# Performance work log

Measured on AMD Instinct MI355X. Metric: run time of the kernel, lower is better.

The kernel has to match this reference:

```python
import jax, jax.numpy as jnp
import numpy as np

N, E, D, H = 4096, 131072, 256, 8
HD = D // H
NEG_INF = -1e30  # stand-in for float('-inf'); avoids inf-inf NaN issues, softmax identical


def _linear(x, W, b):
    return x @ W + b


def setup_inputs() -> dict:
    key = jax.random.key(0)
    ks = jax.random.split(key, 16)
    s = 1.0 / np.sqrt(D)
    inp = {
        "x": jax.random.normal(ks[0], (N, D), jnp.float32),
        "edge_index": jax.random.randint(ks[1], (2, E), 0, N, jnp.int32),
        "edge_attr": jax.random.normal(ks[2], (E, D), jnp.float32),
        "Wq": jax.random.normal(ks[3], (D, D), jnp.float32) * s,
        "bq": jnp.zeros((D,), jnp.float32),
        "Wk": jax.random.normal(ks[4], (D, D), jnp.float32) * s,
        "bk": jnp.zeros((D,), jnp.float32),
        "Wv": jax.random.normal(ks[5], (D, D), jnp.float32) * s,
        "bv": jnp.zeros((D,), jnp.float32),
        "We": jax.random.normal(ks[6], (D, D), jnp.float32) * s,
        "be": jnp.zeros((D,), jnp.float32),
        "Wo": jax.random.normal(ks[7], (D, D), jnp.float32) * s,
        "bo": jnp.zeros((D,), jnp.float32),
        "Wi": jax.random.normal(ks[8], (D, D), jnp.float32) * s,
        "bi": jnp.zeros((D,), jnp.float32),
        "ln_g": jnp.ones((D,), jnp.float32),
        "ln_b": jnp.zeros((D,), jnp.float32),
    }
    return inp


def reference(x, edge_index, edge_attr, Wq, bq, Wk, bk, Wv, bv, We, be, Wo, bo, Wi, bi, ln_g, ln_b):
    n, e = x.shape[0], edge_attr.shape[0]
    Q = _linear(x, Wq, bq).reshape(n, H, HD)
    K = _linear(x, Wk, bk).reshape(n, H, HD)
    V = _linear(x, Wv, bv).reshape(n, H, HD)
    Efeat = _linear(edge_attr, We, be).reshape(e, H, HD)

    src, tgt = edge_index[0], edge_index[1]
    Q_src = Q[src]                     # (E, H, HD)
    K_tgt = K[tgt]                     # (E, H, HD)
    attn_edge = ((Q_src * K_tgt).sum(-1)
                 + (Q_src * Efeat).sum(-1)
                 + (Efeat * K_tgt).sum(-1)) / np.sqrt(HD)   # (E, H)

    attn_scores = jnp.full((n, n, H), NEG_INF, jnp.float32)
    attn_scores = attn_scores.at[src, tgt].set(attn_edge)
    attn_self = (Q * K).sum(-1) / np.sqrt(HD)               # (N, H)
    ar = jnp.arange(n)
    attn_scores = attn_scores.at[ar, ar].set(attn_self)

    attn_weights = jax.nn.softmax(attn_scores, axis=1)      # (N, N, H)
    # dropout in eval mode: identity
    node_out = jnp.einsum('ijh,jhd->ihd', attn_weights, V).reshape(n, -1)
    node_out = _linear(node_out, Wo, bo)

    x_proj = _linear(x, Wi, bi)
    h = x_proj + node_out
    mu = h.mean(-1, keepdims=True)
    var = ((h - mu) ** 2).mean(-1, keepdims=True)
    node_out = (h - mu) / jnp.sqrt(var + 1e-5) * ln_g + ln_b

    edge_out = _linear(edge_attr, We, be)
    return node_out, edge_out
```

## Files before the change

kernel.cpp:

```cpp
#include <hip/hip_runtime.h>

#define N_NODES 4096
#define N_EDGES 131072
#define DIM     256
#define HEADS   8
#define HDIM    32
#define MAXDEG  320
#define MAXDEGP 321

typedef unsigned short u16;
typedef unsigned int   u32;

using f32x4  = __attribute__((ext_vector_type(4))) float;
using bf16x8 = __attribute__((ext_vector_type(8))) short;
using u16x4  = __attribute__((ext_vector_type(4))) unsigned short;
using u16x8  = __attribute__((ext_vector_type(8))) unsigned short;

__device__ __forceinline__ u16 f2bf(float f) {
  u32 u = __float_as_uint(f);
  u += 0x7fffu + ((u >> 16) & 1u);
  return (u16)(u >> 16);
}
__device__ __forceinline__ float bf2f(u16 u) {
  return __uint_as_float(((u32)u) << 16);
}
__device__ __forceinline__ float dot4(float4 a, float4 b) {
  return a.x * b.x + a.y * b.y + a.z * b.z + a.w * b.w;
}

__global__ __launch_bounds__(256) void prep2_k(
    const float* __restrict__ Wq, const float* __restrict__ Wk,
    const float* __restrict__ Wv, const float* __restrict__ Wi,
    const float* __restrict__ We, const float* __restrict__ Wo,
    const float* __restrict__ bq, const float* __restrict__ bk,
    const float* __restrict__ bv, const float* __restrict__ bi,
    u16* __restrict__ WcatT, u16* __restrict__ WeT, u16* __restrict__ WoT,
    float* __restrict__ bcat, int* __restrict__ cursor)
{
  __shared__ float t[64][65];
  int b = blockIdx.x;
  int tid = threadIdx.x;
  if (b < 96) {
    int mat = b >> 4, tile = b & 15;
    int k0 = (tile >> 2) * 64, n0 = (tile & 3) * 64;
    const float* W = (mat == 0) ? Wq : (mat == 1) ? Wk : (mat == 2) ? Wv
                   : (mat == 3) ? Wi : (mat == 4) ? We : Wo;
    u16* dst; int nbase;
    if (mat < 4)      { dst = WcatT; nbase = mat * 256; }
    else if (mat == 4){ dst = WeT;   nbase = 0; }
    else              { dst = WoT;   nbase = 0; }
    int c = tid & 63, r0 = tid >> 6;
#pragma unroll
    for (int r = 0; r < 16; ++r) {
      int row = r0 + r * 4;
      t[row][c] = W[(size_t)(k0 + row) * 256 + n0 + c];
    }
    __syncthreads();
#pragma unroll
    for (int r = 0; r < 16; ++r) {
      int nn = r0 + r * 4;
      dst[(size_t)(nbase + n0 + nn) * 256 + k0 + c] = f2bf(t[c][nn]);
    }
  } else if (b == 96) {
#pragma unroll
    for (int j = 0; j < 4; ++j) {
      const float* bb = (j == 0) ? bq : (j == 1) ? bk : (j == 2) ? bv : bi;
      bcat[j * 256 + tid] = bb[tid];
    }
  } else {
    ((int4*)cursor)[(b - 97) * 256 + tid] = make_int4(0, 0, 0, 0);
  }
}

template<int MODE>
__device__ __forceinline__ void gemm_big_body(
    const float* __restrict__ A, const u16* __restrict__ BT,
    const float* __restrict__ bias, float* __restrict__ C, int Nn,
    int m0, int nc0,
    u16* __restrict__ Kb, u16* __restrict__ Vb,
    const float* __restrict__ QKVI, const float* __restrict__ lng,
    const float* __restrict__ lnb, float* __restrict__ outN,
    u16 (&As)[2][128 * 32], u16 (&Bs)[2][256 * 32])
{
  const int tid = threadIdx.x;
  const int w = tid >> 6, l = tid & 63;
  const int wr = w >> 2, wc = w & 3;
  const int fr = l & 15, hi = l >> 4;

  f32x4 pa[2];
  u16x8 pb[2];
  f32x4 acc[4][4] = {};

  auto loadstep = [&](int kt) {
#pragma unroll
    for (int i = 0; i < 2; ++i) {
      int j = tid + 512 * i;
      pa[i] = __builtin_nontemporal_load(
          (const f32x4*)(A + (size_t)(m0 + (j >> 3)) * 256 + kt * 32 + ((j & 7) << 2)));
    }
#pragma unroll
    for (int i = 0; i < 2; ++i) {
      int j = tid + 512 * i;
      pb[i] = *(const u16x8*)(BT + (size_t)(nc0 + (j >> 2)) * 256 + kt * 32 + ((j & 3) << 3));
    }
  };
  auto storestep = [&](int buf) {
#pragma unroll
    for (int i = 0; i < 2; ++i) {
      int j = tid + 512 * i;
      int row = j >> 3;
      int c16 = (j & 7) >> 1, half = j & 1;
      int swc = (c16 + ((row >> 1) & 3)) & 3;
      u16x4 u;
      u.x = f2bf(pa[i][0]); u.y = f2bf(pa[i][1]); u.z = f2bf(pa[i][2]); u.w = f2bf(pa[i][3]);
      *(u16x4*)&As[buf][row * 32 + swc * 8 + half * 4] = u;
    }
#pragma unroll
    for (int i = 0; i < 2; ++i) {
      int j = tid + 512 * i;
      int row = j >> 2;
      int swc = ((j & 3) + ((row >> 1) & 3)) & 3;
      *(u16x8*)&Bs[buf][row * 32 + swc * 8] = pb[i];
    }
  };

  loadstep(0);
  storestep(0);

#pragma unroll
  for (int kt = 0; kt < 8; ++kt) {
    if (kt < 7) loadstep(kt + 1);
    __builtin_amdgcn_sched_barrier(0);
    asm volatile("s_waitcnt lgkmcnt(0)" ::: "memory");
    __builtin_amdgcn_s_barrier();
    __builtin_amdgcn_sched_barrier(0);
    const int cur = kt & 1;
    bf16x8 a[4], b[4];
#pragma unroll
    for (int mi = 0; mi < 4; ++mi) {
      int rA = wr * 64 + mi * 16 + fr;
      int swc = (hi + ((rA >> 1) & 3)) & 3;
      a[mi] = *(const bf16x8*)&As[cur][rA * 32 + swc * 8];
    }
#pragma unroll
    for (int ni = 0; ni < 4; ++ni) {
      int rB = wc * 64 + ni * 16 + fr;
      int swc = (hi + ((rB >> 1) & 3)) & 3;
      b[ni] = *(const bf16x8*)&Bs[cur][rB * 32 + swc * 8];
    }
#pragma unroll
    for (int mi = 0; mi < 4; ++mi)
#pragma unroll
      for (int ni = 0; ni < 4; ++ni)
        acc[mi][ni] = __builtin_amdgcn_mfma_f32_16x16x32_bf16(
            b[ni], a[mi], acc[mi][ni], 0, 0, 0);
    if (kt < 7) storestep((kt + 1) & 1);
  }

  if constexpr (MODE == 0) {
#pragma unroll
    for (int mi = 0; mi < 4; ++mi) {
      int row = m0 + wr * 64 + mi * 16 + fr;
#pragma unroll
      for (int ni = 0; ni < 4; ++ni) {
        int col = wc * 64 + ni * 16 + hi * 4;
        float4 bv = *(const float4*)&bias[col];
        f32x4 v = acc[mi][ni];
        float4 o;
        o.x = v[0] + bv.x; o.y = v[1] + bv.y; o.z = v[2] + bv.z; o.w = v[3] + bv.w;
        *(float4*)&C[(size_t)row * 256 + col] = o;
      }
    }
  } else if constexpr (MODE == 1) {
#pragma unroll
    for (int mi = 0; mi < 4; ++mi) {
      int row = m0 + wr * 64 + mi * 16 + fr;
#pragma unroll
      for (int ni = 0; ni < 4; ++ni) {
        int col = nc0 + wc * 64 + ni * 16 + hi * 4;
        float4 bv = *(const float4*)&bias[col];
        f32x4 v = acc[mi][ni];
        float4 o;
        o.x = v[0] + bv.x; o.y = v[1] + bv.y; o.z = v[2] + bv.z; o.w = v[3] + bv.w;
        *(float4*)&C[(size_t)row * 1024 + col] = o;
        u16x4 ub;
        ub.x = f2bf(o.x); ub.y = f2bf(o.y); ub.z = f2bf(o.z); ub.w = f2bf(o.w);
        if (nc0 == 256) *(u16x4*)&Kb[(size_t)row * 256 + (col - 256)] = ub;
        if (nc0 == 512) *(u16x4*)&Vb[(size_t)row * 256 + (col - 512)] = ub;
      }
    }
  } else {
    __syncthreads();
    float* s_sum = (float*)&As[0][0];
    float* s_sq  = (float*)&As[1][0];
#pragma unroll
    for (int mi = 0; mi < 4; ++mi) {
      int r = wr * 64 + mi * 16 + fr;
      int row = m0 + r;
      float ps = 0.f, pq = 0.f;
#pragma unroll
      for (int ni = 0; ni < 4; ++ni) {
        int col = wc * 64 + ni * 16 + hi * 4;
        float4 bv = *(const float4*)&bias[col];
        float4 xp = *(const float4*)&QKVI[(size_t)row * 1024 + 768 + col];
        acc[mi][ni][0] += bv.x + xp.x;
        acc[mi][ni][1] += bv.y + xp.y;
        acc[mi][ni][2] += bv.z + xp.z;
        acc[mi][ni][3] += bv.w + xp.w;
#pragma unroll
        for (int j = 0; j < 4; ++j) {
          float vv = acc[mi][ni][j];
          ps += vv; pq += vv * vv;
        }
      }
      s_sum[r * 16 + wc * 4 + hi] = ps;
      s_sq [r * 16 + wc * 4 + hi] = pq;
    }
    __syncthreads();
    float* s_mu = (float*)&Bs[0][0];
    float* s_rs = s_mu + 128;
    if (tid < 128) {
      float s = 0.f, q = 0.f;
#pragma unroll
      for (int k = 0; k < 16; ++k) { s += s_sum[tid * 16 + k]; q += s_sq[tid * 16 + k]; }
      float mu = s * (1.0f / 256.0f);
      float var = q * (1.0f / 256.0f) - mu * mu;
      s_mu[tid] = mu;
      s_rs[tid] = rsqrtf(var + 1e-5f);
    }
    __syncthreads();
#pragma unroll
    for (int mi = 0; mi < 4; ++mi) {
      int r = wr * 64 + mi * 16 + fr;
      int row = m0 + r;
      float mu = s_mu[r], rs = s_rs[r];
#pragma unroll
      for (int ni = 0; ni < 4; ++ni) {
        int col = wc * 64 + ni * 16 + hi * 4;
        float4 g4 = *(const float4*)&lng[col];
        float4 b4 = *(const float4*)&lnb[col];
        float4 o;
        o.x = (acc[mi][ni][0] - mu) * rs * g4.x + b4.x;
        o.y = (acc[mi][ni][1] - mu) * rs * g4.y + b4.y;
        o.z = (acc[mi][ni][2] - mu) * rs * g4.z + b4.z;
        o.w = (acc[mi][ni][3] - mu) * rs * g4.w + b4.w;
        *(float4*)&outN[(size_t)row * 256 + col] = o;
      }
    }
  }
}

__global__ __launch_bounds__(512) void gemm_all_k(
    const float* __restrict__ ea, const u16* __restrict__ WeT,
    const float* __restrict__ be, float* __restrict__ outE,
    const float* __restrict__ x, const u16* __restrict__ WcatT,
    const float* __restrict__ bcat, float* __restrict__ QKVI,
    u16* __restrict__ Kb, u16* __restrict__ Vb)
{
  __shared__ u16 As[2][128 * 32];
  __shared__ u16 Bs[2][256 * 32];
  int bid = blockIdx.x;
  int r = bid % 9, q = bid / 9;
  if (r < 8) {
    int j = q * 8 + r;
    gemm_big_body<0>(ea, WeT, be, outE, 256, j * 128, 0,
                     nullptr, nullptr, nullptr, nullptr, nullptr, nullptr, As, Bs);
  } else {
    gemm_big_body<1>(x, WcatT, bcat, QKVI, 1024, (q >> 2) * 128, (q & 3) * 256,
                     Kb, Vb, nullptr, nullptr, nullptr, nullptr, As, Bs);
  }
}

__global__ __launch_bounds__(512) void gemm_wo_k(
    const float* __restrict__ agg, const u16* __restrict__ WoT,
    const float* __restrict__ bo, const float* __restrict__ QKVI,
    const float* __restrict__ lng, const float* __restrict__ lnb,
    float* __restrict__ outN)
{
  __shared__ u16 As[2][128 * 32];
  __shared__ u16 Bs[2][256 * 32];
  gemm_big_body<2>(agg, WoT, bo, nullptr, 256, blockIdx.x * 128, 0,
                   nullptr, nullptr, QKVI, lng, lnb, outN, As, Bs);
}

__global__ __launch_bounds__(256) void scatter_k(const int* __restrict__ src,
                                                 int* __restrict__ cursor,
                                                 int* __restrict__ slots)
{
  int e = blockIdx.x * 256 + threadIdx.x;
  if (e < N_EDGES) {
    int s = src[e];
    int p = atomicAdd(&cursor[s], 1);
    if (p < MAXDEG) slots[(size_t)s * MAXDEG + p] = e;
  }
}

__global__ __launch_bounds__(256) void node_attn_k(
    const float* __restrict__ QKVI, const float* __restrict__ Ef,
    const u16* __restrict__ Kb, const u16* __restrict__ Vb,
    const int* __restrict__ cursor, const int* __restrict__ slots,
    const int* __restrict__ tgt, float* __restrict__ agg)
{
  __shared__ int   s_eid[MAXDEG];
  __shared__ int   s_tgt[MAXDEG];
  __shared__ float s_sc[HEADS][MAXDEGP];
  __shared__ unsigned char s_alive[MAXDEG];
  __shared__ float s_self[8];
  __shared__ float s_wself[8];

  const float scl = 0.17677669529663687f;
  int i = blockIdx.x;
  int deg = cursor[i];
  if (deg > MAXDEG) deg = MAXDEG;
  int tid = threadIdx.x;
  int w = tid >> 6, l = tid & 63;
  int h = tid >> 5, d = tid & 31;

  for (int t = tid; t < deg; t += 256) {
    int e = slots[(size_t)i * MAXDEG + t];
    s_eid[t] = e;
    s_tgt[t] = tgt[e];
  }
  __syncthreads();

  float4 q4 = *(const float4*)&QKVI[(size_t)i * 1024 + 4 * l];

  if (w == 0) {
    u16x4 kb = *(const u16x4*)&Kb[(size_t)i * 256 + 4 * l];
    float4 k4 = make_float4(bf2f(kb.x), bf2f(kb.y), bf2f(kb.z), bf2f(kb.w));
    float c = dot4(q4, k4);
    c += __shfl_xor(c, 1); c += __shfl_xor(c, 2); c += __shfl_xor(c, 4);
    if ((l & 7) == 0) s_self[l >> 3] = c * scl;
  }

  for (int t0 = w; t0 < deg; t0 += 16) {
    float4 ef[4], k4[4];
#pragma unroll
    for (int u = 0; u < 4; ++u) {
      int t = t0 + 4 * u;
      if (t < deg) {
        ef[u] = *(const float4*)&Ef[(size_t)s_eid[t] * 256 + 4 * l];
        u16x4 kb = *(const u16x4*)&Kb[(size_t)s_tgt[t] * 256 + 4 * l];
        k4[u] = make_float4(bf2f(kb.x), bf2f(kb.y), bf2f(kb.z), bf2f(kb.w));
      }
    }
#pragma unroll
    for (int u = 0; u < 4; ++u) {
      int t = t0 + 4 * u;
      if (t < deg) {
        float c = dot4(q4, ef[u]) + dot4(ef[u], k4[u]) + dot4(q4, k4[u]);
        c += __shfl_xor(c, 1); c += __shfl_xor(c, 2); c += __shfl_xor(c, 4);
        if ((l & 7) == 0) s_sc[l >> 3][t] = c * scl;
      }
    }
  }

  for (int t = tid; t < deg; t += 256) {
    int tt = s_tgt[t], ee = s_eid[t];
    bool alive = (tt != i);
    if (alive)
      for (int u = 0; u < deg; ++u)
        if (s_tgt[u] == tt && s_eid[u] > ee) { alive = false; break; }
    s_alive[t] = alive ? 1 : 0;
  }
  __syncthreads();

  {
    float m = s_self[h];
    for (int t = d; t < deg; t += 32)
      if (s_alive[t]) m = fmaxf(m, s_sc[h][t]);
#pragma unroll
    for (int off = 16; off > 0; off >>= 1) m = fmaxf(m, __shfl_xor(m, off, 32));
    float lsum = 0.f;
    for (int t = d; t < deg; t += 32) {
      float wv = s_alive[t] ? expf(s_sc[h][t] - m) : 0.f;
      s_sc[h][t] = wv;
      lsum += wv;
    }
#pragma unroll
    for (int off = 16; off > 0; off >>= 1) lsum += __shfl_xor(lsum, off, 32);
    float wself = expf(s_self[h] - m);
    float inv = 1.f / (lsum + wself);
    if (d == 0) s_wself[h] = wself * inv;
    for (int t = d; t < deg; t += 32) s_sc[h][t] *= inv;
  }
  __syncthreads();

  int col = tid;
  float accv = s_wself[h] * bf2f(Vb[(size_t)i * 256 + col]);
  int t0 = 0;
  for (; t0 + 4 <= deg; t0 += 4) {
    float vl[4];
#pragma unroll
    for (int u = 0; u < 4; ++u)
      vl[u] = bf2f(Vb[(size_t)s_tgt[t0 + u] * 256 + col]);
#pragma unroll
    for (int u = 0; u < 4; ++u)
      accv += s_sc[h][t0 + u] * vl[u];
  }
  for (; t0 < deg; ++t0)
    accv += s_sc[h][t0] * bf2f(Vb[(size_t)s_tgt[t0] * 256 + col]);
  agg[(size_t)i * 256 + col] = accv;
}

extern "C" void kernel_launch(void* const* d_in, const int* in_sizes, int n_in,
                              void* d_out, int out_size, void* d_ws, size_t ws_size,
                              hipStream_t stream) {
  (void)in_sizes; (void)n_in; (void)out_size; (void)ws_size;
  const float* x  = (const float*)d_in[0];
  const int*   ei = (const int*)d_in[1];
  const float* ea = (const float*)d_in[2];
  const float* Wq = (const float*)d_in[3];  const float* bq = (const float*)d_in[4];
  const float* Wk = (const float*)d_in[5];  const float* bk = (const float*)d_in[6];
  const float* Wv = (const float*)d_in[7];  const float* bv = (const float*)d_in[8];
  const float* We = (const float*)d_in[9];  const float* be = (const float*)d_in[10];
  const float* Wo = (const float*)d_in[11]; const float* bo = (const float*)d_in[12];
  const float* Wi = (const float*)d_in[13]; const float* bi = (const float*)d_in[14];
  const float* lng = (const float*)d_in[15]; const float* lnb = (const float*)d_in[16];

  const int* src = ei;
  const int* tgt = ei + N_EDGES;

  char* ws = (char*)d_ws;
  u16*   WcatT   = (u16*)(ws + 0);
  u16*   WeT     = (u16*)(ws + 524288);
  u16*   WoT     = (u16*)(ws + 655360);
  float* bcat    = (float*)(ws + 786432);
  float* QKVI    = (float*)(ws + 790528);
  int*   cursor  = (int*)(ws + 17567744);
  int*   slots   = (int*)(ws + 17584128);
  float* agg     = (float*)(ws + 22827008);
  u16*   Kb      = (u16*)(ws + 27021312);
  u16*   Vb      = (u16*)(ws + 29118464);

  float* outN = (float*)d_out;
  float* outE = (float*)d_out + (size_t)N_NODES * DIM;

  prep2_k<<<101, 256, 0, stream>>>(Wq, Wk, Wv, Wi, We, Wo, bq, bk, bv, bi,
                                   WcatT, WeT, WoT, bcat, cursor);

  scatter_k<<<N_EDGES / 256, 256, 0, stream>>>(src, cursor, slots);

  gemm_all_k<<<1152, 512, 0, stream>>>(ea, WeT, be, outE, x, WcatT, bcat,
                                       QKVI, Kb, Vb);

  node_attn_k<<<N_NODES, 256, 0, stream>>>(QKVI, outE, Kb, Vb,
                                           cursor, slots, tgt, agg);

  gemm_wo_k<<<N_NODES / 128, 512, 0, stream>>>(agg, WoT, bo, QKVI, lng, lnb, outN);
}
```

Measured before the change: 161.3 us.

## Fuse edge scatter into GEMM launch, store Q as bf16, deepen attention edge batching

Removes the separate scatter kernel and runs the CSR bucketing as the first 256 blocks of the combined GEMM launch, saving one launch and letting the scatter overlap with GEMM tiles. It also stops writing the full fp32 QKVI buffer: Q is stored as bf16 and only the input projection Xp is kept in fp32, which cuts write traffic and the node-attention Q read. The node attention loop now batches 8 edges per warp instead of 4 for more memory-level parallelism, at the cost of more registers. Q in bf16 adds some rounding error to the attention scores.

New measurement: 170.0 us. 1.05x slower.

```diff
diff --git a/kernel.cpp b/kernel.cpp
--- a/kernel.cpp
+++ b/kernel.cpp
@@ -75,10 +75,10 @@
 template<int MODE>
 __device__ __forceinline__ void gemm_big_body(
     const float* __restrict__ A, const u16* __restrict__ BT,
-    const float* __restrict__ bias, float* __restrict__ C, int Nn,
+    const float* __restrict__ bias, float* __restrict__ C,
     int m0, int nc0,
-    u16* __restrict__ Kb, u16* __restrict__ Vb,
-    const float* __restrict__ QKVI, const float* __restrict__ lng,
+    u16* __restrict__ Qb, u16* __restrict__ Kb, u16* __restrict__ Vb,
+    float* __restrict__ Xp, const float* __restrict__ lng,
     const float* __restrict__ lnb, float* __restrict__ outN,
     u16 (&As)[2][128 * 32], u16 (&Bs)[2][256 * 32])
 {
@@ -182,11 +182,12 @@
         f32x4 v = acc[mi][ni];
         float4 o;
         o.x = v[0] + bv.x; o.y = v[1] + bv.y; o.z = v[2] + bv.z; o.w = v[3] + bv.w;
-        *(float4*)&C[(size_t)row * 1024 + col] = o;
         u16x4 ub;
         ub.x = f2bf(o.x); ub.y = f2bf(o.y); ub.z = f2bf(o.z); ub.w = f2bf(o.w);
-        if (nc0 == 256) *(u16x4*)&Kb[(size_t)row * 256 + (col - 256)] = ub;
-        if (nc0 == 512) *(u16x4*)&Vb[(size_t)row * 256 + (col - 512)] = ub;
+        if (nc0 == 0)   *(u16x4*)&Qb[(size_t)row * 256 + col]          = ub;
+        if (nc0 == 256) *(u16x4*)&Kb[(size_t)row * 256 + (col - 256)]  = ub;
+        if (nc0 == 512) *(u16x4*)&Vb[(size_t)row * 256 + (col - 512)]  = ub;
+        if (nc0 == 768) *(float4*)&Xp[(size_t)row * 256 + (col - 768)] = o;
       }
     }
   } else {
@@ -202,7 +203,7 @@
       for (int ni = 0; ni < 4; ++ni) {
         int col = wc * 64 + ni * 16 + hi * 4;
         float4 bv = *(const float4*)&bias[col];
-        float4 xp = *(const float4*)&QKVI[(size_t)row * 1024 + 768 + col];
+        float4 xp = *(const float4*)&Xp[(size_t)row * 256 + col];
         acc[mi][ni][0] += bv.x + xp.x;
         acc[mi][ni][1] += bv.y + xp.y;
         acc[mi][ni][2] += bv.z + xp.z;
@@ -254,49 +255,49 @@
     const float* __restrict__ ea, const u16* __restrict__ WeT,
     const float* __restrict__ be, float* __restrict__ outE,
     const float* __restrict__ x, const u16* __restrict__ WcatT,
-    const float* __restrict__ bcat, float* __restrict__ QKVI,
-    u16* __restrict__ Kb, u16* __restrict__ Vb)
+    const float* __restrict__ bcat,
+    u16* __restrict__ Qb, u16* __restrict__ Kb, u16* __restrict__ Vb,
+    float* __restrict__ Xp,
+    const int* __restrict__ src, int* __restrict__ cursor,
+    int* __restrict__ slots)
 {
   __shared__ u16 As[2][128 * 32];
   __shared__ u16 Bs[2][256 * 32];
   int bid = blockIdx.x;
-  int r = bid % 9, q = bid / 9;
+  if (bid < 256) {
+    int e = bid * 512 + threadIdx.x;
+    int s = src[e];
+    int p = atomicAdd(&cursor[s], 1);
+    if (p < MAXDEG) slots[(size_t)s * MAXDEG + p] = e;
+    return;
+  }
+  int g = bid - 256;
+  int r = g % 9, q = g / 9;
   if (r < 8) {
     int j = q * 8 + r;
-    gemm_big_body<0>(ea, WeT, be, outE, 256, j * 128, 0,
-                     nullptr, nullptr, nullptr, nullptr, nullptr, nullptr, As, Bs);
+    gemm_big_body<0>(ea, WeT, be, outE, j * 128, 0,
+                     nullptr, nullptr, nullptr, nullptr, nullptr, nullptr, nullptr,
+                     As, Bs);
   } else {
-    gemm_big_body<1>(x, WcatT, bcat, QKVI, 1024, (q >> 2) * 128, (q & 3) * 256,
-                     Kb, Vb, nullptr, nullptr, nullptr, nullptr, As, Bs);
+    gemm_big_body<1>(x, WcatT, bcat, nullptr, (q >> 2) * 128, (q & 3) * 256,
+                     Qb, Kb, Vb, Xp, nullptr, nullptr, nullptr, As, Bs);
   }
 }
 
 __global__ __launch_bounds__(512) void gemm_wo_k(
     const float* __restrict__ agg, const u16* __restrict__ WoT,
-    const float* __restrict__ bo, const float* __restrict__ QKVI,
+    const float* __restrict__ bo, float* __restrict__ Xp,
     const float* __restrict__ lng, const float* __restrict__ lnb,
     float* __restrict__ outN)
 {
   __shared__ u16 As[2][128 * 32];
   __shared__ u16 Bs[2][256 * 32];
-  gemm_big_body<2>(agg, WoT, bo, nullptr, 256, blockIdx.x * 128, 0,
-                   nullptr, nullptr, QKVI, lng, lnb, outN, As, Bs);
-}
-
-__global__ __launch_bounds__(256) void scatter_k(const int* __restrict__ src,
-                                                 int* __restrict__ cursor,
-                                                 int* __restrict__ slots)
-{
-  int e = blockIdx.x * 256 + threadIdx.x;
-  if (e < N_EDGES) {
-    int s = src[e];
-    int p = atomicAdd(&cursor[s], 1);
-    if (p < MAXDEG) slots[(size_t)s * MAXDEG + p] = e;
-  }
+  gemm_big_body<2>(agg, WoT, bo, nullptr, blockIdx.x * 128, 0,
+                   nullptr, nullptr, nullptr, Xp, lng, lnb, outN, As, Bs);
 }
 
 __global__ __launch_bounds__(256) void node_attn_k(
-    const float* __restrict__ QKVI, const float* __restrict__ Ef,
+    const u16* __restrict__ Qb, const float* __restrict__ Ef,
     const u16* __restrict__ Kb, const u16* __restrict__ Vb,
     const int* __restrict__ cursor, const int* __restrict__ slots,
     const int* __restrict__ tgt, float* __restrict__ agg)
@@ -323,7 +324,8 @@
   }
   __syncthreads();
 
-  float4 q4 = *(const float4*)&QKVI[(size_t)i * 1024 + 4 * l];
+  u16x4 qb = *(const u16x4*)&Qb[(size_t)i * 256 + 4 * l];
+  float4 q4 = make_float4(bf2f(qb.x), bf2f(qb.y), bf2f(qb.z), bf2f(qb.w));
 
   if (w == 0) {
     u16x4 kb = *(const u16x4*)&Kb[(size_t)i * 256 + 4 * l];
@@ -333,10 +335,10 @@
     if ((l & 7) == 0) s_self[l >> 3] = c * scl;
   }
 
-  for (int t0 = w; t0 < deg; t0 += 16) {
-    float4 ef[4], k4[4];
-#pragma unroll
-    for (int u = 0; u < 4; ++u) {
+  for (int t0 = w; t0 < deg; t0 += 32) {
+    float4 ef[8], k4[8];
+#pragma unroll
+    for (int u = 0; u < 8; ++u) {
       int t = t0 + 4 * u;
       if (t < deg) {
         ef[u] = *(const float4*)&Ef[(size_t)s_eid[t] * 256 + 4 * l];
@@ -345,7 +347,7 @@
       }
     }
 #pragma unroll
-    for (int u = 0; u < 4; ++u) {
+    for (int u = 0; u < 8; ++u) {
       int t = t0 + 4 * u;
       if (t < deg) {
         float c = dot4(q4, ef[u]) + dot4(ef[u], k4[u]) + dot4(q4, k4[u]);
@@ -426,12 +428,13 @@
   u16*   WeT     = (u16*)(ws + 524288);
   u16*   WoT     = (u16*)(ws + 655360);
   float* bcat    = (float*)(ws + 786432);
-  float* QKVI    = (float*)(ws + 790528);
-  int*   cursor  = (int*)(ws + 17567744);
-  int*   slots   = (int*)(ws + 17584128);
-  float* agg     = (float*)(ws + 22827008);
-  u16*   Kb      = (u16*)(ws + 27021312);
-  u16*   Vb      = (u16*)(ws + 29118464);
+  float* Xp      = (float*)(ws + 790528);
+  int*   cursor  = (int*)(ws + 4984832);
+  int*   slots   = (int*)(ws + 5001216);
+  float* agg     = (float*)(ws + 10244096);
+  u16*   Qb      = (u16*)(ws + 14438400);
+  u16*   Kb      = (u16*)(ws + 16535552);
+  u16*   Vb      = (u16*)(ws + 18632704);
 
   float* outN = (float*)d_out;
   float* outE = (float*)d_out + (size_t)N_NODES * DIM;
@@ -439,13 +442,11 @@
   prep2_k<<<101, 256, 0, stream>>>(Wq, Wk, Wv, Wi, We, Wo, bq, bk, bv, bi,
                                    WcatT, WeT, WoT, bcat, cursor);
 
-  scatter_k<<<N_EDGES / 256, 256, 0, stream>>>(src, cursor, slots);
-
-  gemm_all_k<<<1152, 512, 0, stream>>>(ea, WeT, be, outE, x, WcatT, bcat,
-                                       QKVI, Kb, Vb);
-
-  node_attn_k<<<N_NODES, 256, 0, stream>>>(QKVI, outE, Kb, Vb,
+  gemm_all_k<<<1408, 512, 0, stream>>>(ea, WeT, be, outE, x, WcatT, bcat,
+                                       Qb, Kb, Vb, Xp, src, cursor, slots);
+
+  node_attn_k<<<N_NODES, 256, 0, stream>>>(Qb, outE, Kb, Vb,
                                            cursor, slots, tgt, agg);
 
-  gemm_wo_k<<<N_NODES / 128, 512, 0, stream>>>(agg, WoT, bo, QKVI, lng, lnb, outN);
-}
+  gemm_wo_k<<<N_NODES / 128, 512, 0, stream>>>(agg, WoT, bo, Xp, lng, lnb, outN);
+}
```
